# Kernel optimization log

Hardware: AMD Instinct MI355X
Metric: run time of the kernel (lower is better)

## Reference

```python
import jax, jax.numpy as jnp
import numpy as np

LECUN_A = 1.7159
LECUN_B = 0.666


def lecun_tanh(x):
    return LECUN_A * jnp.tanh(LECUN_B * x)


def setup_inputs() -> dict:
    key = jax.random.key(0)
    ks = jax.random.split(key, 12)
    B, T, I, H, U = 128, 1024, 256, 512, 1024
    s_in = 1.0 / np.sqrt(I + H)
    s_u = 1.0 / np.sqrt(U)
    return {
        "input": jax.random.normal(ks[0], (B, T, I), jnp.float32),
        "hx": jax.random.normal(ks[1], (B, T, H), jnp.float32),
        "ts": jax.random.uniform(ks[2], (B, T), jnp.float32),
        "W0": jax.random.normal(ks[3], (I + H, U), jnp.float32) * s_in,
        "b0": jnp.zeros((U,), jnp.float32),
        "W1": jax.random.normal(ks[4], (U, U), jnp.float32) * s_u,
        "b1": jnp.zeros((U,), jnp.float32),
        "W_ff1": jax.random.normal(ks[5], (U, H), jnp.float32) * s_u,
        "b_ff1": jnp.zeros((H,), jnp.float32),
        "W_ff2": jax.random.normal(ks[6], (U, H), jnp.float32) * s_u,
        "b_ff2": jnp.zeros((H,), jnp.float32),
        "W_ta": jax.random.normal(ks[7], (U, H), jnp.float32) * s_u,
        "b_ta": jnp.zeros((H,), jnp.float32),
        "W_tb": jax.random.normal(ks[8], (U, H), jnp.float32) * s_u,
        "b_tb": jnp.zeros((H,), jnp.float32),
    }


def reference(input, hx, ts, W0, b0, W1, b1, W_ff1, b_ff1, W_ff2, b_ff2,
              W_ta, b_ta, W_tb, b_tb):
    # x: [B, T, I+H]
    x = jnp.concatenate([input, hx], axis=2)
    # backbone: Linear -> LeCun -> Linear -> LeCun
    x = lecun_tanh(jnp.einsum("btc,cu->btu", x, W0) + b0)
    x = lecun_tanh(jnp.einsum("btu,uv->btv", x, W1) + b1)
    # four parallel heads sharing x: [B, T, H] each
    ff1 = jnp.tanh(jnp.einsum("btu,uh->bth", x, W_ff1) + b_ff1)
    ff2 = jnp.tanh(jnp.einsum("btu,uh->bth", x, W_ff2) + b_ff2)
    t_a = jnp.einsum("btu,uh->bth", x, W_ta) + b_ta
    t_b = jnp.einsum("btu,uh->bth", x, W_tb) + b_tb
    # time-gated interpolation
    t_interp = jax.nn.sigmoid(t_a * ts[:, :, None] + t_b)
    new_hidden = ff1 * (1.0 - t_interp) + t_interp * ff2
    return new_hidden
```

## Files before the change

kernel.cpp:

```cpp
#include <hip/hip_runtime.h>
#include <hip/hip_bf16.h>


typedef unsigned short u16;
typedef __bf16 bf16x8_t __attribute__((ext_vector_type(8)));
typedef float f32x4_t __attribute__((ext_vector_type(4)));
typedef u16 u16x8_t __attribute__((ext_vector_type(8)));

#define M_TOTAL 131072

__device__ __forceinline__ u16 f2bf(float f) {
  union { float f; unsigned u; } v; v.f = f;
  unsigned r = v.u + 0x7FFFu + ((v.u >> 16) & 1u);
  return (u16)(r >> 16);
}

__device__ __forceinline__ float fast_tanh(float x) {
  x = fminf(15.f, fmaxf(-15.f, x));
  float e = __expf(2.f * x);
  return (e - 1.f) * __builtin_amdgcn_rcpf(e + 1.f);
}

__device__ __forceinline__ float fast_sigmoid(float x) {
  return __builtin_amdgcn_rcpf(1.f + __expf(-x));
}

__device__ __forceinline__ void gload_lds16(const void* g, void* l) {
  __builtin_amdgcn_global_load_lds(
      (const __attribute__((address_space(1))) unsigned int*)g,
      (__attribute__((address_space(3))) unsigned int*)l,
      16, 0, 0);
}


__global__ void prep_x(const float* __restrict__ inp, const float* __restrict__ hx,
                       u16* __restrict__ X) {
  const int total = M_TOTAL * 96;
  int stride = gridDim.x * blockDim.x;
  for (int v = blockIdx.x * blockDim.x + threadIdx.x; v < total; v += stride) {
    int m = v / 96; int c = v - m * 96;
    const float* src = (c < 32) ? (inp + (size_t)m * 256 + (c << 3))
                                : (hx + (size_t)m * 512 + ((size_t)(c - 32) << 3));
    f32x4_t a = *(const f32x4_t*)src;
    f32x4_t b = *(const f32x4_t*)(src + 4);
    u16x8_t o;
    o[0]=f2bf(a[0]); o[1]=f2bf(a[1]); o[2]=f2bf(a[2]); o[3]=f2bf(a[3]);
    o[4]=f2bf(b[0]); o[5]=f2bf(b[1]); o[6]=f2bf(b[2]); o[7]=f2bf(b[3]);
    *(u16x8_t*)(X + (size_t)m * 768 + (c << 3)) = o;
  }
}

__global__ void prep_w(const float* __restrict__ W0, const float* __restrict__ W1,
                       const float* __restrict__ Wf1, const float* __restrict__ Wf2,
                       const float* __restrict__ Wta, const float* __restrict__ Wtb,
                       const float* __restrict__ bf1, const float* __restrict__ bf2,
                       const float* __restrict__ bta, const float* __restrict__ btb,
                       u16* __restrict__ W0P, u16* __restrict__ W1P,
                       u16* __restrict__ WhP, float* __restrict__ biasi) {
  int id = blockIdx.x * blockDim.x + threadIdx.x;
  u16x8_t o;
  if (id < 98304) {
    int l = id & 63, r = id >> 6;
    int g = r % 64, t = r / 64;
    int col = g * 16 + (l & 15), kb = t * 32 + ((l >> 4) << 3);
#pragma unroll
    for (int e = 0; e < 8; ++e) o[e] = f2bf(W0[(size_t)(kb + e) * 1024 + col]);
    *((u16x8_t*)W0P + id) = o;
  } else if (id < 229376) {
    int id2 = id - 98304;
    int l = id2 & 63, r = id2 >> 6;
    int g = r & 63, t = r >> 6;
    int col = g * 16 + (l & 15), kb = t * 32 + ((l >> 4) << 3);
#pragma unroll
    for (int e = 0; e < 8; ++e) o[e] = f2bf(W1[(size_t)(kb + e) * 1024 + col]);
    *((u16x8_t*)W1P + id2) = o;
  } else if (id < 491520) {
    int id3 = id - 229376;
    int l = id3 & 63, r = id3 >> 6;
    int g = r & 127, t = r >> 7;
    int head = g & 3;
    int n = (g >> 2) * 16 + (l & 15), kb = t * 32 + ((l >> 4) << 3);
    const float* W = (head == 0) ? Wf1 : (head == 1) ? Wf2 : (head == 2) ? Wta : Wtb;
#pragma unroll
    for (int e = 0; e < 8; ++e) o[e] = f2bf(W[(size_t)(kb + e) * 512 + n]);
    *((u16x8_t*)WhP + id3) = o;
  } else if (id < 492032) {
    int h = id - 491520;
    int base = ((h >> 4) << 6) + (h & 15);
    biasi[base +  0] = bf1[h];
    biasi[base + 16] = bf2[h];
    biasi[base + 32] = bta[h];
    biasi[base + 48] = btb[h];
  }
}


#define BARX()   do { __builtin_amdgcn_s_barrier(); __builtin_amdgcn_sched_barrier(0); } while(0)
#define LGKM0()  do { asm volatile("s_waitcnt lgkmcnt(0)" ::: "memory"); __builtin_amdgcn_sched_barrier(0); } while(0)
#define SCHEDB() __builtin_amdgcn_sched_barrier(0)
#define WAITVM_(n) do { asm volatile("s_waitcnt vmcnt(" #n ")" ::: "memory"); __builtin_amdgcn_sched_barrier(0); } while(0)
#define WAITVM(n) WAITVM_(n)

template<int K, int NI, int EPI>
__global__ __launch_bounds__(512, 2)
void gemmC(const u16* __restrict__ A, const char* __restrict__ Bp,
           const float* __restrict__ bias, const float* __restrict__ ts,
           void* __restrict__ Cout)
{
  constexpr int NTn = NI / 256;
  constexpr int G64 = NI / 16;
  constexpr size_t G64K = (size_t)G64 * 1024;
  constexpr int NT = K / 32;
  constexpr int NWG = (M_TOTAL / 256) * NTn;
  __shared__ __align__(16) char smem[65536];

  const int bid = ((blockIdx.x & 7) * (NWG >> 3)) + (blockIdx.x >> 3);
  const int mt = bid / NTn, nt = bid % NTn;
  const int tileM = mt * 256, tileN = nt * 256;

  const int tid = threadIdx.x, w = tid >> 6, l = tid & 63;
  const int wm = w >> 2, wn = w & 3;

  const int laneK = ((l & 3) << 3) ^ (((l >> 5) & 1) << 4);
  const u16* aS0 = A + (size_t)(tileM + 32 * w + (l >> 2)) * K + laneK;
  const u16* aS1 = aS0 + (size_t)16 * K;
  char* ldsW = smem + (w << 11);
  const int colRs = ((l >> 4) << 4) ^ (((l >> 3) & 1) << 5);
  const char* aRd = smem + (wm * 128 + (l & 15)) * 64 + colRs;
  const char* bp0 = Bp + ((size_t)(((tileN >> 4) + wn * 4) * 64 + l) << 4);

  f32x4_t acc[8][4];
#pragma unroll
  for (int i = 0; i < 8; ++i)
#pragma unroll
    for (int j = 0; j < 4; ++j) acc[i][j] = f32x4_t{0.f, 0.f, 0.f, 0.f};

  bf16x8_t af[8], ba[4], bb[4];

#define LDB(BK, OFF) do { \
    BK[0] = *(const bf16x8_t*)(bp0 + (OFF)); \
    BK[1] = *(const bf16x8_t*)(bp0 + (OFF) + 1024); \
    BK[2] = *(const bf16x8_t*)(bp0 + (OFF) + 2048); \
    BK[3] = *(const bf16x8_t*)(bp0 + (OFF) + 3072); } while(0)

#define GSTEP(W1N, SLOT, BK, DOST, TOFF, DOBL, BLOFF) do { \
    WAITVM(W1N); BARX(); \
    if (DOST) { \
      gload_lds16(aS0 + (TOFF), ldsW + (((SLOT) + 3) & 3) * 16384); \
      gload_lds16(aS1 + (TOFF), ldsW + (((SLOT) + 3) & 3) * 16384 + 1024); \
    } \
    _Pragma("unroll") for (int m_ = 0; m_ < 8; ++m_) \
      af[m_] = *(const bf16x8_t*)(aRd + (SLOT) * 16384 + m_ * 1024); \
    LGKM0(); \
    __builtin_amdgcn_s_setprio(1); \
    _Pragma("unroll") for (int m_ = 0; m_ < 8; ++m_) \
      _Pragma("unroll") for (int n_ = 0; n_ < 4; ++n_) \
        acc[m_][n_] = __builtin_amdgcn_mfma_f32_16x16x32_bf16( \
            af[m_], BK[n_], acc[m_][n_], 0, 0, 0); \
    __builtin_amdgcn_s_setprio(0); \
    SCHEDB(); \
    if (DOBL) LDB(BK, BLOFF); \
    SCHEDB(); \
  } while(0)

  LDB(ba, 0);
  LDB(bb, G64K);
  SCHEDB();
  gload_lds16(aS0,      ldsW);
  gload_lds16(aS1,      ldsW + 1024);
  gload_lds16(aS0 + 32, ldsW + 16384);
  gload_lds16(aS1 + 32, ldsW + 16384 + 1024);
  gload_lds16(aS0 + 64, ldsW + 32768);
  gload_lds16(aS1 + 64, ldsW + 32768 + 1024);
  SCHEDB();

  GSTEP(4,  0, ba, 1, 3 * 32, 1, 2 * G64K);
  GSTEP(8,  1, bb, 1, 4 * 32, 1, 3 * G64K);
  GSTEP(12, 2, ba, 1, 5 * 32, 1, 4 * G64K);
  GSTEP(16, 3, bb, 1, 6 * 32, 1, 5 * G64K);

  {
    size_t tOff = 7 * 32;
    size_t blOff = 6 * G64K;
#pragma unroll 1
    for (int it = 0; it < (NT - 8) / 4; ++it) {
      GSTEP(16, 0, ba, 1, tOff,      1, blOff);
      GSTEP(16, 1, bb, 1, tOff + 32, 1, blOff + G64K);
      GSTEP(16, 2, ba, 1, tOff + 64, 1, blOff + 2 * G64K);
      GSTEP(16, 3, bb, 1, tOff + 96, 1, blOff + 3 * G64K);
      tOff += 128; blOff += 4 * G64K;
    }
  }

  GSTEP(16, 0, ba, 1, (size_t)(NT - 1) * 32, 1, (size_t)(NT - 2) * G64K);
  GSTEP(16, 1, bb, 0, 0, 1, (size_t)(NT - 1) * G64K);
  GSTEP(14, 2, ba, 0, 0, 0, 0);
  GSTEP(8,  3, bb, 0, 0, 0, 0);

  const int colBase = tileN + wn * 64 + (l & 15);
  float bv[4];
  bv[0] = bias[colBase];      bv[1] = bias[colBase + 16];
  bv[2] = bias[colBase + 32]; bv[3] = bias[colBase + 48];

  if constexpr (EPI == 0) {
    u16* C = (u16*)Cout;
    const int rowB = tileM + wm * 128 + ((l >> 4) << 2);
#pragma unroll
    for (int m = 0; m < 8; ++m)
#pragma unroll
      for (int nn = 0; nn < 4; ++nn)
#pragma unroll
        for (int j = 0; j < 4; ++j) {
          float v = acc[m][nn][j] + bv[nn];
          float t = 1.7159f * fast_tanh(0.666f * v);
          C[(size_t)(rowB + m * 16 + j) * NI + colBase + nn * 16] = f2bf(t);
        }
  } else {
    const int hg = ((tileN + wn * 64) >> 6) * 16 + (l & 15);
    float* out = (float*)Cout;
#pragma unroll
    for (int m = 0; m < 8; ++m)
#pragma unroll
      for (int j = 0; j < 4; ++j) {
        const int rl = wm * 128 + m * 16 + ((l >> 4) << 2) + j;
        const float tsv = ts[tileM + rl];
        float ff1 = fast_tanh(acc[m][0][j] + bv[0]);
        float ff2 = fast_tanh(acc[m][1][j] + bv[1]);
        float s = fast_sigmoid((acc[m][2][j] + bv[2]) * tsv + (acc[m][3][j] + bv[3]));
        out[(size_t)(tileM + rl) * 512 + hg] = ff1 + s * (ff2 - ff1);
      }
  }
#undef LDB
#undef GSTEP
}


extern "C" void kernel_launch(void* const* d_in, const int* in_sizes, int n_in,
                              void* d_out, int out_size, void* d_ws, size_t ws_size,
                              hipStream_t stream) {
  const float* input = (const float*)d_in[0];
  const float* hx    = (const float*)d_in[1];
  const float* ts    = (const float*)d_in[2];
  const float* W0    = (const float*)d_in[3];
  const float* b0    = (const float*)d_in[4];
  const float* W1    = (const float*)d_in[5];
  const float* b1    = (const float*)d_in[6];
  const float* Wff1  = (const float*)d_in[7];
  const float* bff1  = (const float*)d_in[8];
  const float* Wff2  = (const float*)d_in[9];
  const float* bff2  = (const float*)d_in[10];
  const float* Wta   = (const float*)d_in[11];
  const float* bta   = (const float*)d_in[12];
  const float* Wtb   = (const float*)d_in[13];
  const float* btb   = (const float*)d_in[14];

  const size_t WS_NEEDED = 544743424ull;
  if (ws_size < WS_NEEDED) return;
  char* ws = (char*)d_ws;
  u16* Xcat = (u16*)(ws);
  u16* X2   = (u16*)(ws);
  u16* X1   = (u16*)(ws + 268435456ull);
  u16* W0P  = (u16*)(ws + 536870912ull);
  u16* W1P  = (u16*)(ws + 538443776ull);
  u16* WhP  = (u16*)(ws + 540540928ull);
  float* biasi = (float*)(ws + 544735232ull);

  prep_x<<<2048, 256, 0, stream>>>(input, hx, Xcat);
  prep_w<<<1922, 256, 0, stream>>>(W0, W1, Wff1, Wff2, Wta, Wtb,
                                   bff1, bff2, bta, btb, W0P, W1P, WhP, biasi);

  gemmC<768, 1024, 0><<<2048, 512, 0, stream>>>(Xcat, (const char*)W0P, b0, nullptr, X1);
  gemmC<1024, 1024, 0><<<2048, 512, 0, stream>>>(X1, (const char*)W1P, b1, nullptr, X2);
  gemmC<1024, 2048, 1><<<4096, 512, 0, stream>>>(X2, (const char*)WhP, biasi, ts, d_out);
}
```

Before: 1.221 ms.

## Restructure GEMM pipeline into two-K-tile regions with 6-slot LDS ring

Replaces the per-K-tile step, which had one barrier and waitcnt for every 32-wide K tile, with regions that each cover two K tiles behind a single barrier. LDS grows to 96KB as a ring of six slots, with two tiles in flight ahead of the tiles being consumed. The aim is to halve barrier and synchronisation overhead and to keep more global-to-LDS traffic outstanding. The cost is more LDS per block, which may cut occupancy under launch_bounds(512,2), and the explicit lgkmcnt wait is dropped in favour of compiler-inserted waits.

```diff
diff --git a/kernel.cpp b/kernel.cpp
--- a/kernel.cpp
+++ b/kernel.cpp
@@ -95,11 +95,12 @@
 }
 
 
-#define BARX()   do { __builtin_amdgcn_s_barrier(); __builtin_amdgcn_sched_barrier(0); } while(0)
-#define LGKM0()  do { asm volatile("s_waitcnt lgkmcnt(0)" ::: "memory"); __builtin_amdgcn_sched_barrier(0); } while(0)
 #define SCHEDB() __builtin_amdgcn_sched_barrier(0)
-#define WAITVM_(n) do { asm volatile("s_waitcnt vmcnt(" #n ")" ::: "memory"); __builtin_amdgcn_sched_barrier(0); } while(0)
-#define WAITVM(n) WAITVM_(n)
+#define RSYNC_(n) do { \
+    asm volatile("s_waitcnt vmcnt(" #n ")" ::: "memory"); \
+    __builtin_amdgcn_s_barrier(); \
+    __builtin_amdgcn_sched_barrier(0); } while(0)
+#define RSYNC(n) RSYNC_(n)
 
 template<int K, int NI, int EPI>
 __global__ __launch_bounds__(512, 2)
@@ -111,8 +112,9 @@
   constexpr int G64 = NI / 16;
   constexpr size_t G64K = (size_t)G64 * 1024;
   constexpr int NT = K / 32;
+  constexpr int NRG = NT / 2;
   constexpr int NWG = (M_TOTAL / 256) * NTn;
-  __shared__ __align__(16) char smem[65536];
+  __shared__ __align__(16) char smem[98304];
 
   const int bid = ((blockIdx.x & 7) * (NWG >> 3)) + (blockIdx.x >> 3);
   const int mt = bid / NTn, nt = bid % NTn;
@@ -143,24 +145,33 @@
     BK[2] = *(const bf16x8_t*)(bp0 + (OFF) + 2048); \
     BK[3] = *(const bf16x8_t*)(bp0 + (OFF) + 3072); } while(0)
 
-#define GSTEP(W1N, SLOT, BK, DOST, TOFF, DOBL, BLOFF) do { \
-    WAITVM(W1N); BARX(); \
-    if (DOST) { \
-      gload_lds16(aS0 + (TOFF), ldsW + (((SLOT) + 3) & 3) * 16384); \
-      gload_lds16(aS1 + (TOFF), ldsW + (((SLOT) + 3) & 3) * 16384 + 1024); \
-    } \
-    _Pragma("unroll") for (int m_ = 0; m_ < 8; ++m_) \
-      af[m_] = *(const bf16x8_t*)(aRd + (SLOT) * 16384 + m_ * 1024); \
-    LGKM0(); \
+#define MFMAQ(BK) do { \
     __builtin_amdgcn_s_setprio(1); \
     _Pragma("unroll") for (int m_ = 0; m_ < 8; ++m_) \
       _Pragma("unroll") for (int n_ = 0; n_ < 4; ++n_) \
         acc[m_][n_] = __builtin_amdgcn_mfma_f32_16x16x32_bf16( \
             af[m_], BK[n_], acc[m_][n_], 0, 0, 0); \
-    __builtin_amdgcn_s_setprio(0); \
-    SCHEDB(); \
-    if (DOBL) LDB(BK, BLOFF); \
-    SCHEDB(); \
+    __builtin_amdgcn_s_setprio(0); } while(0)
+
+#define REGION(WV, DOST, DOB) do { \
+    RSYNC(WV); \
+    int stOff_ = rdOff + 65536; if (stOff_ >= 98304) stOff_ -= 98304; \
+    if (DOST) { \
+      gload_lds16(aS0 + tOff,      ldsW + stOff_); \
+      gload_lds16(aS1 + tOff,      ldsW + stOff_ + 1024); \
+      gload_lds16(aS0 + tOff + 32, ldsW + stOff_ + 16384); \
+      gload_lds16(aS1 + tOff + 32, ldsW + stOff_ + 16384 + 1024); \
+    } \
+    _Pragma("unroll") for (int m_ = 0; m_ < 8; ++m_) \
+      af[m_] = *(const bf16x8_t*)(aRd + rdOff + m_ * 1024); \
+    MFMAQ(ba); \
+    if (DOB) LDB(ba, bOff); \
+    _Pragma("unroll") for (int m_ = 0; m_ < 8; ++m_) \
+      af[m_] = *(const bf16x8_t*)(aRd + rdOff + 16384 + m_ * 1024); \
+    MFMAQ(bb); \
+    if (DOB) LDB(bb, bOff + G64K); \
+    rdOff += 32768; if (rdOff >= 98304) rdOff -= 98304; \
+    tOff += 64; bOff += 2 * G64K; \
   } while(0)
 
   LDB(ba, 0);
@@ -172,30 +183,19 @@
   gload_lds16(aS1 + 32, ldsW + 16384 + 1024);
   gload_lds16(aS0 + 64, ldsW + 32768);
   gload_lds16(aS1 + 64, ldsW + 32768 + 1024);
+  gload_lds16(aS0 + 96, ldsW + 49152);
+  gload_lds16(aS1 + 96, ldsW + 49152 + 1024);
   SCHEDB();
 
-  GSTEP(4,  0, ba, 1, 3 * 32, 1, 2 * G64K);
-  GSTEP(8,  1, bb, 1, 4 * 32, 1, 3 * G64K);
-  GSTEP(12, 2, ba, 1, 5 * 32, 1, 4 * G64K);
-  GSTEP(16, 3, bb, 1, 6 * 32, 1, 5 * G64K);
-
-  {
-    size_t tOff = 7 * 32;
-    size_t blOff = 6 * G64K;
+  int rdOff = 0;
+  size_t tOff = 128;
+  size_t bOff = 2 * G64K;
+
+  REGION(4, true, true);
 #pragma unroll 1
-    for (int it = 0; it < (NT - 8) / 4; ++it) {
-      GSTEP(16, 0, ba, 1, tOff,      1, blOff);
-      GSTEP(16, 1, bb, 1, tOff + 32, 1, blOff + G64K);
-      GSTEP(16, 2, ba, 1, tOff + 64, 1, blOff + 2 * G64K);
-      GSTEP(16, 3, bb, 1, tOff + 96, 1, blOff + 3 * G64K);
-      tOff += 128; blOff += 4 * G64K;
-    }
-  }
-
-  GSTEP(16, 0, ba, 1, (size_t)(NT - 1) * 32, 1, (size_t)(NT - 2) * G64K);
-  GSTEP(16, 1, bb, 0, 0, 1, (size_t)(NT - 1) * G64K);
-  GSTEP(14, 2, ba, 0, 0, 0, 0);
-  GSTEP(8,  3, bb, 0, 0, 0, 0);
+  for (int t = 1; t <= NRG - 3; ++t) REGION(12, true, true);
+  REGION(12, false, true);
+  REGION(8, false, false);
 
   const int colBase = tileN + wn * 64 + (l & 15);
   float bv[4];
@@ -231,7 +231,8 @@
       }
   }
 #undef LDB
-#undef GSTEP
+#undef MFMAQ
+#undef REGION
 }
 
 
```

After: 1.293 ms. 5.9% more time.
